# Performance work log

Hardware: AMD Instinct MI355X
Metric: run time of the kernel (lower is better)

## Reference

```python
import jax, jax.numpy as jnp
import numpy as np

B, L, D, H = 2, 1024, 1024, 16
HD = D // H  # head_dim = 64


def setup_inputs() -> dict:
    key = jax.random.key(0)
    ks = jax.random.split(key, 6)
    s = 1.0 / np.sqrt(D)
    return {
        "x": jax.random.normal(ks[0], (B, L, D), jnp.float32),
        "structure_bias": jax.random.normal(ks[1], (B, L, D), jnp.float32),
        # weights stored as [in, out] (transposed vs torch nn.Linear)
        "Wqkv": jax.random.normal(ks[2], (D, 3 * D), jnp.float32) * s,
        "bqkv": jnp.zeros((3 * D,), jnp.float32),
        "Ws": jax.random.normal(ks[3], (D, D), jnp.float32) * s,
        "bs": jnp.zeros((D,), jnp.float32),
        "Wo": jax.random.normal(ks[4], (D, D), jnp.float32) * s,
        "bo": jnp.zeros((D,), jnp.float32),
    }


def reference(x, structure_bias, Wqkv, bqkv, Ws, bs, Wo, bo):
    b, l, d = x.shape
    # qkv: [B, L, 3, H, HD] -> (3, B, H, L, HD)
    qkv = (x @ Wqkv + bqkv).reshape(b, l, 3, H, HD).transpose(2, 0, 3, 1, 4)
    q, k, v = qkv[0], qkv[1], qkv[2]
    scale = 1.0 / jnp.sqrt(jnp.float32(HD))
    attn = jnp.einsum("bhld,bhmd->bhlm", q, k) * scale  # [B,H,L,L]
    # structure bias: Linear then view(B, 1, L, L); requires L == feature_dim
    sw = (structure_bias @ Ws + bs).reshape(b, 1, l, l)
    attn = jax.nn.softmax(attn + sw, axis=-1)
    out = jnp.einsum("bhlm,bhmd->bhld", attn, v)  # [B,H,L,HD]
    out = out.transpose(0, 2, 1, 3).reshape(b, l, d)
    return out @ Wo + bo
```

## Files before the change

kernel.cpp:

```cpp
#include <hip/hip_runtime.h>
#include <stdint.h>
#include <stddef.h>


typedef float f32x4 __attribute__((ext_vector_type(4)));
typedef short s16x8 __attribute__((ext_vector_type(8)));
typedef unsigned short u16x8 __attribute__((ext_vector_type(8)));
typedef unsigned short u16x4 __attribute__((ext_vector_type(4)));

__device__ inline unsigned short f2bf(float f) {
    unsigned u = __builtin_bit_cast(unsigned, f);
    u += 0x7fffu + ((u >> 16) & 1u);
    return (unsigned short)(u >> 16);
}

__device__ inline f32x4 mfma16(s16x8 a, s16x8 b, f32x4 c) {
    return __builtin_amdgcn_mfma_f32_16x16x32_bf16(a, b, c, 0, 0, 0);
}

__device__ inline void gld_lds16(const void* g, const void* lds_base) {
    __builtin_amdgcn_global_load_lds(
        (const __attribute__((address_space(1))) void*)(uintptr_t)g,
        (__attribute__((address_space(3))) void*)(unsigned)(uintptr_t)lds_base,
        16, 0, 0);
}

__global__ __launch_bounds__(256) void prep_k(const float* __restrict__ x,
                                              const float* __restrict__ sb,
                                              const float* __restrict__ Wqkv,
                                              const float* __restrict__ Ws,
                                              const float* __restrict__ Wo,
                                              unsigned short* __restrict__ xb,
                                              unsigned short* __restrict__ sbb,
                                              unsigned short* __restrict__ wqkvt,
                                              unsigned short* __restrict__ wst,
                                              unsigned short* __restrict__ wot) {
    __shared__ float tile[64][65];
    const int blk = blockIdx.x, t = threadIdx.x;
    if (blk < 2048) {
        const float* src = (blk < 1024) ? x : sb;
        unsigned short* dst = (blk < 1024) ? xb : sbb;
        int i = (blk & 1023) * 256 + t;
        const float4* s4 = (const float4*)src;
        float4 a = s4[2 * i], b = s4[2 * i + 1];
        u16x8 o;
        o[0] = f2bf(a.x); o[1] = f2bf(a.y); o[2] = f2bf(a.z); o[3] = f2bf(a.w);
        o[4] = f2bf(b.x); o[5] = f2bf(b.y); o[6] = f2bf(b.z); o[7] = f2bf(b.w);
        *(u16x8*)(dst + (size_t)i * 8) = o;
        return;
    }
    int tt = blk - 2048;
    const float* W; unsigned short* Wt; int N, n0, k0;
    if (tt < 768)       { W = Wqkv; Wt = wqkvt; N = 3072; n0 = (tt % 48) * 64; k0 = (tt / 48) * 64; }
    else if (tt < 1024) { tt -= 768;  W = Ws; Wt = wst; N = 1024; n0 = (tt & 15) * 64; k0 = (tt >> 4) * 64; }
    else                { tt -= 1024; W = Wo; Wt = wot; N = 1024; n0 = (tt & 15) * 64; k0 = (tt >> 4) * 64; }
    const int lr = t >> 4, lc = (t & 15) * 4;
#pragma unroll
    for (int rr = 0; rr < 4; rr++) {
        int r = lr + rr * 16;
        float4 v = *(const float4*)(W + (size_t)(k0 + r) * N + n0 + lc);
        tile[r][lc] = v.x; tile[r][lc + 1] = v.y; tile[r][lc + 2] = v.z; tile[r][lc + 3] = v.w;
    }
    __syncthreads();
    const int wn = t >> 3, wk = (t & 7) * 8;
#pragma unroll
    for (int rr = 0; rr < 2; rr++) {
        int n = wn + rr * 32;
        u16x8 o;
#pragma unroll
        for (int j = 0; j < 8; j++) o[j] = f2bf(tile[wk + j][n]);
        *(u16x8*)(Wt + (size_t)(n0 + n) * 1024 + k0 + wk) = o;
    }
}

__global__ __launch_bounds__(256, 2) void gemm01_k(const unsigned short* __restrict__ xb,
                                                   const unsigned short* __restrict__ wqkvt,
                                                   const float* __restrict__ bqkv,
                                                   const unsigned short* __restrict__ sbb,
                                                   const unsigned short* __restrict__ wst,
                                                   const float* __restrict__ bs,
                                                   unsigned short* __restrict__ q,
                                                   unsigned short* __restrict__ kk_,
                                                   unsigned short* __restrict__ vt,
                                                   float* __restrict__ swf) {
    __shared__ unsigned short lA[2][8192];
    __shared__ unsigned short lB[2][8192];
    const int blk = blockIdx.x, t = threadIdx.x;
    const int wave = t >> 6, lane = t & 63, c = lane & 15, g = lane >> 4;
    const int wr = (wave >> 1) * 64, wc = (wave & 1) * 64;

    const unsigned short* A;
    const unsigned short* Bt;
    const float* bias;
    int bn0, bm0, epi;
    if (blk < 384) { A = xb;  Bt = wqkvt; bias = bqkv; epi = 0;
                     bn0 = (blk % 24) * 128; bm0 = (blk / 24) * 128; }
    else           { int bb = blk - 384; A = sbb; Bt = wst; bias = bs; epi = 1;
                     bn0 = (bb & 7) * 128; bm0 = (bb >> 3) * 128; }

    size_t aoff[4], boff[4];
#pragma unroll
    for (int j = 0; j < 4; j++) {
        int s = j * 256 + t, row = s >> 3, ch = (s & 7) ^ (row & 7);
        aoff[j] = (size_t)(bm0 + row) * 1024 + ch * 8;
        boff[j] = (size_t)(bn0 + row) * 1024 + ch * 8;
    }
    char* lAb0 = (char*)lA[0]; char* lBb0 = (char*)lB[0];

#define GS128(buf, kt)                                                                    \
    do {                                                                                  \
        _Pragma("unroll")                                                                 \
        for (int j = 0; j < 4; j++)                                                       \
            gld_lds16(A + aoff[j] + (kt), lAb0 + (buf) * 16384 + j * 4096 + wave * 1024); \
        _Pragma("unroll")                                                                 \
        for (int j = 0; j < 4; j++)                                                       \
            gld_lds16(Bt + boff[j] + (kt), lBb0 + (buf) * 16384 + j * 4096 + wave * 1024);\
    } while (0)

    f32x4 acc[4][4];
#pragma unroll
    for (int i = 0; i < 4; i++)
#pragma unroll
        for (int j = 0; j < 4; j++) acc[i][j] = {0.f, 0.f, 0.f, 0.f};

    GS128(0, 0);
    for (int ks = 0; ks < 16; ++ks) {
        __syncthreads();
        if (ks < 15) GS128((ks + 1) & 1, (ks + 1) * 64);
        const char* aB = lAb0 + (ks & 1) * 16384;
        const char* bB = lBb0 + (ks & 1) * 16384;
#pragma unroll
        for (int kk2 = 0; kk2 < 2; ++kk2) {
            s16x8 af[4], bfr[4];
#pragma unroll
            for (int i = 0; i < 4; i++) {
                int r_ = wr + i * 16 + c;
                af[i] = *(const s16x8*)(aB + r_ * 128 + (((kk2 * 4 + g) ^ (r_ & 7)) << 4));
            }
#pragma unroll
            for (int j = 0; j < 4; j++) {
                int r_ = wc + j * 16 + c;
                bfr[j] = *(const s16x8*)(bB + r_ * 128 + (((kk2 * 4 + g) ^ (r_ & 7)) << 4));
            }
            __builtin_amdgcn_s_setprio(1);
#pragma unroll
            for (int i = 0; i < 4; i++)
#pragma unroll
                for (int j = 0; j < 4; j++)
                    acc[i][j] = mfma16(af[i], bfr[j], acc[i][j]);
            __builtin_amdgcn_s_setprio(0);
        }
    }
#undef GS128

#pragma unroll
    for (int i = 0; i < 4; i++) {
#pragma unroll
        for (int j = 0; j < 4; j++) {
            const int n = bn0 + wc + j * 16 + c;
            const float bv = bias[n];
#pragma unroll
            for (int r = 0; r < 4; r++) {
                const int m = bm0 + wr + i * 16 + g * 4 + r;
                float v = acc[i][j][r] + bv;
                if (epi == 0) {
                    const int sel = n >> 10, h = (n >> 6) & 15, d = n & 63;
                    const int b_ = m >> 10, l_ = m & 1023;
                    const size_t bh = (size_t)((b_ << 4) + h);
                    unsigned short hv = f2bf(v);
                    if (sel == 0)      q[(bh * 1024 + l_) * 64 + d] = hv;
                    else if (sel == 1) kk_[(bh * 1024 + l_) * 64 + d] = hv;
                    else               vt[(bh * 64 + d) * 1024 + l_] = hv;
                } else {
                    swf[(size_t)m * 1024 + n] = v;
                }
            }
        }
    }
}

__global__ __launch_bounds__(256, 3) void gemmo_k(const unsigned short* __restrict__ A,
                                                  const unsigned short* __restrict__ Bt,
                                                  const float* __restrict__ bias,
                                                  float* __restrict__ outf) {
    __shared__ unsigned short lA[2][4096];
    __shared__ unsigned short lB[2][8192];
    const int t = threadIdx.x;
    const int wave = t >> 6, lane = t & 63, c = lane & 15, g = lane >> 4;
    const int bn0 = blockIdx.x * 128, bm0 = blockIdx.y * 64;
    const int wc = wave * 32;

    size_t aoff[2], boff[4];
#pragma unroll
    for (int j = 0; j < 2; j++) {
        int s = j * 256 + t, row = s >> 3, ch = (s & 7) ^ (row & 7);
        aoff[j] = (size_t)(bm0 + row) * 1024 + ch * 8;
    }
#pragma unroll
    for (int j = 0; j < 4; j++) {
        int s = j * 256 + t, row = s >> 3, ch = (s & 7) ^ (row & 7);
        boff[j] = (size_t)(bn0 + row) * 1024 + ch * 8;
    }
    char* lAb0 = (char*)lA[0]; char* lBb0 = (char*)lB[0];

#define GSTAGE(buf, kt)                                                                  \
    do {                                                                                 \
        _Pragma("unroll")                                                                \
        for (int j = 0; j < 2; j++)                                                      \
            gld_lds16(A + aoff[j] + (kt), lAb0 + (buf) * 8192 + j * 4096 + wave * 1024); \
        _Pragma("unroll")                                                                \
        for (int j = 0; j < 4; j++)                                                      \
            gld_lds16(Bt + boff[j] + (kt), lBb0 + (buf) * 16384 + j * 4096 + wave * 1024);\
    } while (0)

    f32x4 acc[4][2];
#pragma unroll
    for (int i = 0; i < 4; i++)
#pragma unroll
        for (int j = 0; j < 2; j++) acc[i][j] = {0.f, 0.f, 0.f, 0.f};

    GSTAGE(0, 0);
    for (int ks = 0; ks < 16; ++ks) {
        __syncthreads();
        if (ks < 15) GSTAGE((ks + 1) & 1, (ks + 1) * 64);
        const char* aB = lAb0 + (ks & 1) * 8192;
        const char* bB = lBb0 + (ks & 1) * 16384;
#pragma unroll
        for (int kk2 = 0; kk2 < 2; ++kk2) {
            s16x8 af[4], bfr[2];
#pragma unroll
            for (int i = 0; i < 4; i++) {
                int r_ = i * 16 + c;
                af[i] = *(const s16x8*)(aB + r_ * 128 + (((kk2 * 4 + g) ^ (r_ & 7)) << 4));
            }
#pragma unroll
            for (int j = 0; j < 2; j++) {
                int r_ = wc + j * 16 + c;
                bfr[j] = *(const s16x8*)(bB + r_ * 128 + (((kk2 * 4 + g) ^ (r_ & 7)) << 4));
            }
            __builtin_amdgcn_s_setprio(1);
#pragma unroll
            for (int i = 0; i < 4; i++)
#pragma unroll
                for (int j = 0; j < 2; j++)
                    acc[i][j] = mfma16(af[i], bfr[j], acc[i][j]);
            __builtin_amdgcn_s_setprio(0);
        }
    }
#undef GSTAGE

#pragma unroll
    for (int i = 0; i < 4; i++) {
#pragma unroll
        for (int j = 0; j < 2; j++) {
            const int n = bn0 + wc + j * 16 + c;
            const float bv = bias[n];
#pragma unroll
            for (int r = 0; r < 4; r++) {
                const int m = bm0 + i * 16 + g * 4 + r;
                outf[(size_t)m * 1024 + n] = acc[i][j][r] + bv;
            }
        }
    }
}

__global__ __launch_bounds__(256, 2) void attn_k(const unsigned short* __restrict__ q,
                                                 const unsigned short* __restrict__ k,
                                                 const unsigned short* __restrict__ vt,
                                                 const float* __restrict__ sw,
                                                 unsigned short* __restrict__ ctx) {
    __shared__ unsigned short kbuf[2][4096];
    __shared__ unsigned short vbuf[2][4096];
    __shared__ unsigned short lP[4][640];
    const int t = threadIdx.x, wave = t >> 6, lane = t & 63, c = lane & 15, g = lane >> 4;
    const int blk = blockIdx.x;
    const int qt = blk & 15, bh = blk >> 4, b_ = bh >> 4, h = bh & 15;
    const int qr = qt * 64 + wave * 16;

    const unsigned short* qbase = q + ((size_t)bh * 1024 + qr) * 64;
    s16x8 qf0 = *(const s16x8*)(qbase + (size_t)c * 64 + g * 8);
    s16x8 qf1 = *(const s16x8*)(qbase + (size_t)c * 64 + 32 + g * 8);

    const unsigned short* kg = k + (size_t)bh * 65536;
    const unsigned short* vg = vt + (size_t)bh * 65536;
    const float* swrow = sw + ((size_t)b_ * 1024 + qr + c) * 1024;

    const int s0 = wave * 128 + lane, s1 = s0 + 64;
    const int r0 = s0 >> 3, ch0 = (s0 & 7) ^ (r0 & 7);
    const int r1 = s1 >> 3, ch1 = (s1 & 7) ^ (r1 & 7);

    const float SC  = 0.125f * 1.4426950408889634f;
    const float L2E = 1.4426950408889634f;
    const float SHIFT = 16.0f;

    const short one_bf = (short)0x3F80;
    const s16x8 ones = { one_bf, one_bf, one_bf, one_bf, one_bf, one_bf, one_bf, one_bf };

    f32x4 acc[4];
    f32x4 accl = {0.f, 0.f, 0.f, 0.f};
#pragma unroll
    for (int nf = 0; nf < 4; nf++) acc[nf] = {0.f, 0.f, 0.f, 0.f};
    unsigned short* wp = lP[wave];
    const int swz = (c & 7);

#define STAGE(buf, kv0)                                                                     \
    do {                                                                                    \
        gld_lds16(kg + (size_t)((kv0) + r0) * 64 + ch0 * 8, (char*)kbuf[buf] + wave * 2048);            \
        gld_lds16(kg + (size_t)((kv0) + r1) * 64 + ch1 * 8, (char*)kbuf[buf] + wave * 2048 + 1024);     \
        gld_lds16(vg + (size_t)r0 * 1024 + (kv0) + ch0 * 8, (char*)vbuf[buf] + wave * 2048);            \
        gld_lds16(vg + (size_t)r1 * 1024 + (kv0) + ch1 * 8, (char*)vbuf[buf] + wave * 2048 + 1024);     \
    } while (0)

    STAGE(0, 0);
    __syncthreads();

    int cur = 0;
    for (int it = 0; it < 16; ++it) {
        const int kv0 = it * 64;
        if (it < 15) STAGE(cur ^ 1, kv0 + 64);
        float4 sws[4];
#pragma unroll
        for (int j = 0; j < 4; j++) sws[j] = *(const float4*)(swrow + kv0 + j * 16 + 4 * g);

        const char* kB = (const char*)kbuf[cur];
        const char* vB = (const char*)vbuf[cur];
#pragma unroll
        for (int ks2 = 0; ks2 < 2; ++ks2) {
            s16x8 kc0 = *(const s16x8*)(kB + ((ks2 * 32 + c) << 7) + (((0 + g) ^ swz) << 4));
            s16x8 kc1 = *(const s16x8*)(kB + ((ks2 * 32 + c) << 7) + (((4 + g) ^ swz) << 4));
            s16x8 kc2 = *(const s16x8*)(kB + ((ks2 * 32 + 16 + c) << 7) + (((0 + g) ^ swz) << 4));
            s16x8 kc3 = *(const s16x8*)(kB + ((ks2 * 32 + 16 + c) << 7) + (((4 + g) ^ swz) << 4));

            __builtin_amdgcn_s_setprio(1);
            f32x4 ss0 = {0.f, 0.f, 0.f, 0.f}, ss1 = {0.f, 0.f, 0.f, 0.f};
            ss0 = mfma16(kc0, qf0, ss0); ss0 = mfma16(kc1, qf1, ss0);
            ss1 = mfma16(kc2, qf0, ss1); ss1 = mfma16(kc3, qf1, ss1);
            __builtin_amdgcn_s_setprio(0);

            float4 swa = sws[2 * ks2], swb = sws[2 * ks2 + 1];
            float p0[4], p1[4];
#pragma unroll
            for (int r = 0; r < 4; r++) {
                float z0 = ss0[r] * SC + ((&swa.x)[r] * L2E - SHIFT);
                float z1 = ss1[r] * SC + ((&swb.x)[r] * L2E - SHIFT);
                p0[r] = __builtin_amdgcn_exp2f(z0);
                p1[r] = __builtin_amdgcn_exp2f(z1);
            }

            u16x4 w0, w1;
#pragma unroll
            for (int r = 0; r < 4; r++) { w0[r] = f2bf(p0[r]); w1[r] = f2bf(p1[r]); }
            *(u16x4*)(wp + c * 40 + 4 * g) = w0;
            *(u16x4*)(wp + c * 40 + 16 + 4 * g) = w1;
            s16x8 ap = *(const s16x8*)((const char*)wp + c * 80 + g * 16);

            __builtin_amdgcn_s_setprio(1);
            accl = mfma16(ones, ap, accl);
#pragma unroll
            for (int nf = 0; nf < 4; nf++) {
                s16x8 vf = *(const s16x8*)(vB + ((nf * 16 + c) << 7) + ((((ks2 << 2) + g) ^ swz) << 4));
                acc[nf] = mfma16(vf, ap, acc[nf]);
            }
            __builtin_amdgcn_s_setprio(0);
        }
        __syncthreads();
        cur ^= 1;
    }
#undef STAGE

    float inv = 1.0f / accl[0];
#pragma unroll
    for (int nf = 0; nf < 4; nf++)
#pragma unroll
        for (int r = 0; r < 4; r++) acc[nf][r] *= inv;

    __syncthreads();
    float* scr = (wave < 2) ? ((float*)kbuf + wave * 1088)
                            : ((float*)vbuf + (wave - 2) * 1088);
#pragma unroll
    for (int nf = 0; nf < 4; nf++)
#pragma unroll
        for (int r = 0; r < 4; r++)
            scr[(nf * 16 + 4 * g + r) * 17 + c] = acc[nf][r];
    __syncthreads();
    u16x8 o0, o1;
#pragma unroll
    for (int j = 0; j < 8; j++) o0[j] = f2bf(scr[(g * 16 + j) * 17 + c]);
#pragma unroll
    for (int j = 0; j < 8; j++) o1[j] = f2bf(scr[(g * 16 + 8 + j) * 17 + c]);
    unsigned short* dst = ctx + ((size_t)(b_ << 10) + qr + c) * 1024 + (h << 6) + g * 16;
    *(u16x8*)dst = o0;
    *(u16x8*)(dst + 8) = o1;
}

extern "C" void kernel_launch(void* const* d_in, const int* in_sizes, int n_in,
                              void* d_out, int out_size, void* d_ws, size_t ws_size,
                              hipStream_t stream) {
    const float* x    = (const float*)d_in[0];
    const float* sb   = (const float*)d_in[1];
    const float* Wqkv = (const float*)d_in[2];
    const float* bqkv = (const float*)d_in[3];
    const float* Ws   = (const float*)d_in[4];
    const float* bs   = (const float*)d_in[5];
    const float* Wo   = (const float*)d_in[6];
    const float* bo   = (const float*)d_in[7];
    float* out = (float*)d_out;

    char* ws = (char*)d_ws;
    unsigned short* xb    = (unsigned short*)(ws);
    unsigned short* sbb   = (unsigned short*)(ws + ((size_t)4 << 20));
    unsigned short* wqkvt = (unsigned short*)(ws + ((size_t)8 << 20));
    unsigned short* wst   = (unsigned short*)(ws + ((size_t)14 << 20));
    unsigned short* wot   = (unsigned short*)(ws + ((size_t)16 << 20));
    unsigned short* qb    = (unsigned short*)(ws + ((size_t)18 << 20));
    unsigned short* kb    = (unsigned short*)(ws + ((size_t)22 << 20));
    unsigned short* vtb   = (unsigned short*)(ws + ((size_t)26 << 20));
    float*          swf   = (float*)        (ws + ((size_t)30 << 20));
    unsigned short* ctxb  = (unsigned short*)(ws + ((size_t)38 << 20));

    prep_k<<<dim3(3328), dim3(256), 0, stream>>>(x, sb, Wqkv, Ws, Wo,
                                                 xb, sbb, wqkvt, wst, wot);
    gemm01_k<<<dim3(512), dim3(256), 0, stream>>>(xb, wqkvt, bqkv, sbb, wst, bs,
                                                  qb, kb, vtb, swf);
    attn_k<<<dim3(512), dim3(256), 0, stream>>>(qb, kb, vtb, swf, ctxb);
    gemmo_k<<<dim3(8, 32), dim3(256), 0, stream>>>(ctxb, wot, bo, out);
}
```

Measured before the change: 83.71 us.

## Split attention KV range across two wave groups per block and merge partials

Doubles the attention block to 512 threads. Two groups of four waves each process half of the key/value sequence (512 keys each) for the same 64 query rows, then group 1 writes partial numerators and denominators to shared memory for group 0 to combine. This works because the softmax uses a fixed shift instead of a running max. The aim is to halve the serial KV loop length per wave and raise occupancy and latency hiding. In exchange it doubles LDS usage per block and adds a reduction step with extra barriers.

```diff
diff --git a/kernel.cpp b/kernel.cpp
--- a/kernel.cpp
+++ b/kernel.cpp
@@ -264,28 +264,29 @@
     }
 }
 
-__global__ __launch_bounds__(256, 2) void attn_k(const unsigned short* __restrict__ q,
+__global__ __launch_bounds__(512, 4) void attn_k(const unsigned short* __restrict__ q,
                                                  const unsigned short* __restrict__ k,
                                                  const unsigned short* __restrict__ vt,
                                                  const float* __restrict__ sw,
                                                  unsigned short* __restrict__ ctx) {
-    __shared__ unsigned short kbuf[2][4096];
-    __shared__ unsigned short vbuf[2][4096];
-    __shared__ unsigned short lP[4][640];
+    __shared__ unsigned short kbuf[2][2][4096];
+    __shared__ unsigned short vbuf[2][2][4096];
+    __shared__ unsigned short lP[8][640];
     const int t = threadIdx.x, wave = t >> 6, lane = t & 63, c = lane & 15, g = lane >> 4;
+    const int grp = wave >> 2, wl = wave & 3;
     const int blk = blockIdx.x;
     const int qt = blk & 15, bh = blk >> 4, b_ = bh >> 4, h = bh & 15;
-    const int qr = qt * 64 + wave * 16;
+    const int qr = qt * 64 + wl * 16;
 
     const unsigned short* qbase = q + ((size_t)bh * 1024 + qr) * 64;
     s16x8 qf0 = *(const s16x8*)(qbase + (size_t)c * 64 + g * 8);
     s16x8 qf1 = *(const s16x8*)(qbase + (size_t)c * 64 + 32 + g * 8);
 
-    const unsigned short* kg = k + (size_t)bh * 65536;
-    const unsigned short* vg = vt + (size_t)bh * 65536;
-    const float* swrow = sw + ((size_t)b_ * 1024 + qr + c) * 1024;
-
-    const int s0 = wave * 128 + lane, s1 = s0 + 64;
+    const unsigned short* kg  = k + (size_t)bh * 65536 + (size_t)grp * 512 * 64;
+    const unsigned short* vgb = vt + (size_t)bh * 65536 + grp * 512;
+    const float* swrow = sw + ((size_t)b_ * 1024 + qr + c) * 1024 + grp * 512;
+
+    const int s0 = wl * 128 + lane, s1 = s0 + 64;
     const int r0 = s0 >> 3, ch0 = (s0 & 7) ^ (r0 & 7);
     const int r1 = s1 >> 3, ch1 = (s1 & 7) ^ (r1 & 7);
 
@@ -303,27 +304,30 @@
     unsigned short* wp = lP[wave];
     const int swz = (c & 7);
 
+    char* kgrp = (char*)kbuf + grp * 16384;
+    char* vgrp = (char*)vbuf + grp * 16384;
+
 #define STAGE(buf, kv0)                                                                     \
     do {                                                                                    \
-        gld_lds16(kg + (size_t)((kv0) + r0) * 64 + ch0 * 8, (char*)kbuf[buf] + wave * 2048);            \
-        gld_lds16(kg + (size_t)((kv0) + r1) * 64 + ch1 * 8, (char*)kbuf[buf] + wave * 2048 + 1024);     \
-        gld_lds16(vg + (size_t)r0 * 1024 + (kv0) + ch0 * 8, (char*)vbuf[buf] + wave * 2048);            \
-        gld_lds16(vg + (size_t)r1 * 1024 + (kv0) + ch1 * 8, (char*)vbuf[buf] + wave * 2048 + 1024);     \
+        gld_lds16(kg + (size_t)((kv0) + r0) * 64 + ch0 * 8, kgrp + (buf) * 8192 + wl * 2048);          \
+        gld_lds16(kg + (size_t)((kv0) + r1) * 64 + ch1 * 8, kgrp + (buf) * 8192 + wl * 2048 + 1024);   \
+        gld_lds16(vgb + (size_t)r0 * 1024 + (kv0) + ch0 * 8, vgrp + (buf) * 8192 + wl * 2048);         \
+        gld_lds16(vgb + (size_t)r1 * 1024 + (kv0) + ch1 * 8, vgrp + (buf) * 8192 + wl * 2048 + 1024);  \
     } while (0)
 
     STAGE(0, 0);
     __syncthreads();
 
     int cur = 0;
-    for (int it = 0; it < 16; ++it) {
+    for (int it = 0; it < 8; ++it) {
         const int kv0 = it * 64;
-        if (it < 15) STAGE(cur ^ 1, kv0 + 64);
+        if (it < 7) STAGE(cur ^ 1, kv0 + 64);
         float4 sws[4];
 #pragma unroll
         for (int j = 0; j < 4; j++) sws[j] = *(const float4*)(swrow + kv0 + j * 16 + 4 * g);
 
-        const char* kB = (const char*)kbuf[cur];
-        const char* vB = (const char*)vbuf[cur];
+        const char* kB = kgrp + cur * 8192;
+        const char* vB = vgrp + cur * 8192;
 #pragma unroll
         for (int ks2 = 0; ks2 < 2; ++ks2) {
             s16x8 kc0 = *(const s16x8*)(kB + ((ks2 * 32 + c) << 7) + (((0 + g) ^ swz) << 4));
@@ -368,29 +372,44 @@
     }
 #undef STAGE
 
-    float inv = 1.0f / accl[0];
-#pragma unroll
-    for (int nf = 0; nf < 4; nf++)
-#pragma unroll
-        for (int r = 0; r < 4; r++) acc[nf][r] *= inv;
-
+    float* pscr = (float*)vbuf;
+    if (grp == 1) {
+        float* pw = pscr + wl * 1040;
+#pragma unroll
+        for (int nf = 0; nf < 4; nf++)
+#pragma unroll
+            for (int r = 0; r < 4; r++)
+                pw[(nf * 16 + 4 * g + r) * 16 + c] = acc[nf][r];
+        if (g == 0) pw[1024 + c] = accl[0];
+    }
     __syncthreads();
-    float* scr = (wave < 2) ? ((float*)kbuf + wave * 1088)
-                            : ((float*)vbuf + (wave - 2) * 1088);
-#pragma unroll
-    for (int nf = 0; nf < 4; nf++)
-#pragma unroll
-        for (int r = 0; r < 4; r++)
-            scr[(nf * 16 + 4 * g + r) * 17 + c] = acc[nf][r];
+
+    float* scr = (float*)kbuf + wl * 1088;
+    if (grp == 0) {
+        float* pw = pscr + wl * 1040;
+#pragma unroll
+        for (int nf = 0; nf < 4; nf++)
+#pragma unroll
+            for (int r = 0; r < 4; r++)
+                acc[nf][r] += pw[(nf * 16 + 4 * g + r) * 16 + c];
+        float inv = 1.0f / (accl[0] + pw[1024 + c]);
+#pragma unroll
+        for (int nf = 0; nf < 4; nf++)
+#pragma unroll
+            for (int r = 0; r < 4; r++)
+                scr[(nf * 16 + 4 * g + r) * 17 + c] = acc[nf][r] * inv;
+    }
     __syncthreads();
-    u16x8 o0, o1;
-#pragma unroll
-    for (int j = 0; j < 8; j++) o0[j] = f2bf(scr[(g * 16 + j) * 17 + c]);
-#pragma unroll
-    for (int j = 0; j < 8; j++) o1[j] = f2bf(scr[(g * 16 + 8 + j) * 17 + c]);
-    unsigned short* dst = ctx + ((size_t)(b_ << 10) + qr + c) * 1024 + (h << 6) + g * 16;
-    *(u16x8*)dst = o0;
-    *(u16x8*)(dst + 8) = o1;
+    if (grp == 0) {
+        u16x8 o0, o1;
+#pragma unroll
+        for (int j = 0; j < 8; j++) o0[j] = f2bf(scr[(g * 16 + j) * 17 + c]);
+#pragma unroll
+        for (int j = 0; j < 8; j++) o1[j] = f2bf(scr[(g * 16 + 8 + j) * 17 + c]);
+        unsigned short* dst = ctx + ((size_t)(b_ << 10) + qr + c) * 1024 + (h << 6) + g * 16;
+        *(u16x8*)dst = o0;
+        *(u16x8*)(dst + 8) = o1;
+    }
 }
 
 extern "C" void kernel_launch(void* const* d_in, const int* in_sizes, int n_in,
@@ -422,6 +441,6 @@
                                                  xb, sbb, wqkvt, wst, wot);
     gemm01_k<<<dim3(512), dim3(256), 0, stream>>>(xb, wqkvt, bqkv, sbb, wst, bs,
                                                   qb, kb, vtb, swf);
-    attn_k<<<dim3(512), dim3(256), 0, stream>>>(qb, kb, vtb, swf, ctxb);
+    attn_k<<<dim3(512), dim3(512), 0, stream>>>(qb, kb, vtb, swf, ctxb);
     gemmo_k<<<dim3(8, 32), dim3(256), 0, stream>>>(ctxb, wot, bo, out);
 }
```

New measurement: 81.35 us. 2.8% less time.
